# Performance work log

Measured on AMD Instinct MI355X. Metric: run time of the kernel, lower is better.

Reference implementation:

```python
import jax, jax.numpy as jnp
import numpy as np

B, S, IN, HID, HEADS, TRAITS = 128, 32, 32, 128, 8, 10


def setup_inputs() -> dict:
    key = jax.random.key(0)
    ks = jax.random.split(key, 40)
    f32 = jnp.float32
    def W(k, shape, s=0.02):
        return (jax.random.normal(k, shape, f32) * s)
    path = jax.random.normal(ks[0], (B, S, IN), f32)
    # monotonically increasing shared time grid (timestamps[0] is what cdeint uses)
    dt = jax.random.uniform(ks[1], (S,), f32, 0.05, 0.15)
    ts = jnp.broadcast_to(jnp.cumsum(dt), (B, S))
    inp = {
        "interaction_path": path,
        "timestamps": ts,
        # initial encoder: Linear(IN,HID) -> LN -> GELU -> Linear(HID,HID) -> LN
        "enc_W1": W(ks[2], (IN, HID)), "enc_b1": jnp.zeros((HID,), f32),
        "enc_g1": jnp.ones((HID,), f32), "enc_bt1": jnp.zeros((HID,), f32),
        "enc_W2": W(ks[3], (HID, HID)), "enc_b2": jnp.zeros((HID,), f32),
        "enc_g2": jnp.ones((HID,), f32), "enc_bt2": jnp.zeros((HID,), f32),
        # vector field: Linear(HID,2HID)->LN->GELU -> Linear(2HID,2HID)->LN->GELU -> Linear(2HID,HID*IN)
        "vf_W1": W(ks[4], (HID, 2 * HID)), "vf_b1": jnp.zeros((2 * HID,), f32),
        "vf_g1": jnp.ones((2 * HID,), f32), "vf_bt1": jnp.zeros((2 * HID,), f32),
        "vf_W2": W(ks[5], (2 * HID, 2 * HID)), "vf_b2": jnp.zeros((2 * HID,), f32),
        "vf_g2": jnp.ones((2 * HID,), f32), "vf_bt2": jnp.zeros((2 * HID,), f32),
        "vf_W3": W(ks[6], (2 * HID, HID * IN), 0.005), "vf_b3": jnp.zeros((HID * IN,), f32),
        # MultiheadAttention (q=k=v, single token)
        "Wq": W(ks[7], (HID, HID)), "bq": jnp.zeros((HID,), f32),
        "Wk": W(ks[8], (HID, HID)), "bk": jnp.zeros((HID,), f32),
        "Wv": W(ks[9], (HID, HID)), "bv": jnp.zeros((HID,), f32),
        "Wo": W(ks[10], (HID, HID)), "bo": jnp.zeros((HID,), f32),
        # trait decoder (2-layer MLP -> TRAITS)
        "dec_W1": W(ks[11], (HID, HID)), "dec_b1": jnp.zeros((HID,), f32),
        "dec_W2": W(ks[12], (HID, TRAITS)), "dec_b2": jnp.zeros((TRAITS,), f32),
    }
    return inp


def reference(interaction_path, timestamps,
              enc_W1, enc_b1, enc_g1, enc_bt1, enc_W2, enc_b2, enc_g2, enc_bt2,
              vf_W1, vf_b1, vf_g1, vf_bt1, vf_W2, vf_b2, vf_g2, vf_bt2, vf_W3, vf_b3,
              Wq, bq, Wk, bk, Wv, bv, Wo, bo,
              dec_W1, dec_b1, dec_W2, dec_b2):
    b, s, in_dim = interaction_path.shape
    hid = enc_W1.shape[1]
    nh = HEADS
    dh = hid // nh

    def ln(x, g, bb):
        mu = jnp.mean(x, -1, keepdims=True)
        v = jnp.mean((x - mu) ** 2, -1, keepdims=True)
        return (x - mu) / jnp.sqrt(v + 1e-5) * g + bb

    gelu = lambda x: jax.nn.gelu(x, approximate=False)

    # initial encoder on first time point (dropout = eval mode)
    x0 = interaction_path[:, 0]
    h0 = gelu(ln(x0 @ enc_W1 + enc_b1, enc_g1, enc_bt1))
    z0 = ln(h0 @ enc_W2 + enc_b2, enc_g2, enc_bt2)  # [B, HID]

    # linear-interpolation control path: piecewise-constant derivative per interval
    dts = timestamps[:, 1:] - timestamps[:, :-1]                       # [B, S-1]
    dX = (interaction_path[:, 1:] - interaction_path[:, :-1]) / dts[..., None]  # [B, S-1, IN]

    def vf(z):
        h = gelu(ln(z @ vf_W1 + vf_b1, vf_g1, vf_bt1))
        h = gelu(ln(h @ vf_W2 + vf_b2, vf_g2, vf_bt2))
        return (h @ vf_W3 + vf_b3).reshape(z.shape[0], hid, in_dim)    # [B, HID, IN]

    def drift(z, dxdt):
        return jnp.einsum('bhi,bi->bh', vf(z), dxdt)

    def rk4_step(z, inp):
        dxdt, hstep = inp               # [B, IN], [B]
        hb = hstep[:, None]
        k1 = drift(z, dxdt)
        k2 = drift(z + 0.5 * hb * k1, dxdt)
        k3 = drift(z + 0.5 * hb * k2, dxdt)
        k4 = drift(z + hb * k3, dxdt)
        z_next = z + (hb / 6.0) * (k1 + 2 * k2 + 2 * k3 + k4)
        return z_next, None

    zT, _ = jax.lax.scan(rk4_step, z0, (jnp.swapaxes(dX, 0, 1), dts.T))  # [B, HID]

    # single-token self-attention (softmax over one key -> weights = 1)
    q = (zT @ Wq + bq).reshape(b, nh, dh)
    k = (zT @ Wk + bk).reshape(b, nh, dh)
    v = (zT @ Wv + bv).reshape(b, nh, dh)
    scores = jnp.sum(q * k, -1, keepdims=True) / jnp.sqrt(jnp.float32(dh))  # [B, nh, 1]
    w = jax.nn.softmax(scores[..., None], axis=-1)                           # [B, nh, 1, 1] == 1
    attn = (w[..., 0] * v).reshape(b, hid)
    final = attn @ Wo + bo
    attention_weights = jnp.mean(w, axis=1)  # [B, 1, 1] averaged over heads (torch default)

    hD = gelu(final @ dec_W1 + dec_b1)
    traits = hD @ dec_W2 + dec_b2            # [B, TRAITS]
    return traits, attention_weights
```

## Files before the change

### kernel.cpp

```cpp
#include <hip/hip_runtime.h>
#include <hip/hip_bf16.h>

#define BB 128
#define SS 32
#define NSTEP 31
#define IND 32
#define HID 128
#define HID2 256

typedef unsigned short u16;
typedef unsigned int u32;
typedef _Float16 f16;
typedef f16 h2 __attribute__((ext_vector_type(2)));
typedef __fp16 fp16v2 __attribute__((ext_vector_type(2)));
typedef _Float16 f16x8 __attribute__((ext_vector_type(8)));
typedef float f32x4 __attribute__((ext_vector_type(4)));

__device__ __forceinline__ float dot2f(u32 a, u32 b, float c){
#if __has_builtin(__builtin_amdgcn_fdot2)
  h2 ha, hb; __builtin_memcpy(&ha, &a, 4); __builtin_memcpy(&hb, &b, 4);
  return __builtin_amdgcn_fdot2(ha, hb, c, false);
#else
  h2 ha, hb; __builtin_memcpy(&ha, &a, 4); __builtin_memcpy(&hb, &b, 4);
  return c + (float)ha[0]*(float)hb[0] + (float)ha[1]*(float)hb[1];
#endif
}
__device__ __forceinline__ u32 pkh2(float a, float b){
  fp16v2 r = __builtin_amdgcn_cvt_pkrtz(a, b);
  u32 u; __builtin_memcpy(&u, &r, 4); return u;
}
__device__ __forceinline__ u16 f2h(float f){ f16 h = (f16)f; u16 u; __builtin_memcpy(&u, &h, 2); return u; }
__device__ __forceinline__ float gelu_f(float x){ return 0.5f * x * (1.0f + erff(x * 0.70710678118654752440f)); }
__device__ __forceinline__ void setprio_hi(){
#if __has_builtin(__builtin_amdgcn_s_setprio)
  __builtin_amdgcn_s_setprio(3);
#endif
}
__device__ __forceinline__ void setprio_lo(){
#if __has_builtin(__builtin_amdgcn_s_setprio)
  __builtin_amdgcn_s_setprio(0);
#endif
}

__device__ __forceinline__ float wred(float v){
  int iv; float tf;
  #define DPPADD(CTRL, RMASK) \
    __builtin_memcpy(&iv, &v, 4); \
    iv = __builtin_amdgcn_update_dpp(0, iv, CTRL, RMASK, 0xf, true); \
    __builtin_memcpy(&tf, &iv, 4); \
    v += tf;
  DPPADD(0x111, 0xf)
  DPPADD(0x112, 0xf)
  DPPADD(0x114, 0xf)
  DPPADD(0x118, 0xf)
  DPPADD(0x142, 0xa)
  DPPADD(0x143, 0xc)
  #undef DPPADD
  return v;
}

__device__ __forceinline__ void bsum2(float x, float y, float* red, int tid, float& ox, float& oy){
  #pragma unroll
  for (int off = 32; off >= 1; off >>= 1){ x += __shfl_xor(x, off); y += __shfl_xor(y, off); }
  __syncthreads();
  if ((tid & 63) == 0){ red[(tid >> 6)*2] = x; red[(tid >> 6)*2 + 1] = y; }
  __syncthreads();
  ox = red[0] + red[2] + red[4] + red[6];
  oy = red[1] + red[3] + red[5] + red[7];
}

__global__ __launch_bounds__(256) void setup_kernel(const float* __restrict__ path,
                                                    const float* __restrict__ ts,
                                                    const float* __restrict__ b3,
                                                    const float* __restrict__ W3,
                                                    const float* __restrict__ W1,
                                                    const float* __restrict__ W2,
                                                    u32* __restrict__ dxh,
                                                    float* __restrict__ hb,
                                                    float* __restrict__ gb,
                                                    u32* __restrict__ w3h,
                                                    u32* __restrict__ w1f,
                                                    u32* __restrict__ w2f){
  const int blk = blockIdx.x, tid = threadIdx.x;
  if (blk < BB){
    const int b = blk;
    __shared__ float sdxp[NSTEP * IND];
    for (int t = tid; t < NSTEP * IND; t += 256){
      int s = t >> 5, i = t & 31;
      float dt = ts[b*SS + s + 1] - ts[b*SS + s];
      sdxp[t] = (path[(b*SS + s + 1)*IND + i] - path[(b*SS + s)*IND + i]) / dt;
    }
    if (tid < NSTEP) hb[b*NSTEP + tid] = ts[b*SS + tid + 1] - ts[b*SS + tid];
    __syncthreads();
    for (int t = tid; t < NSTEP * 16; t += 256){
      int s = t >> 4, i2 = t & 15;
      dxh[((size_t)b*NSTEP + s)*16 + i2] = pkh2(sdxp[s*IND + 2*i2], sdxp[s*IND + 2*i2 + 1]);
    }
    if (tid < HID){
      float w[IND];
      #pragma unroll
      for (int i = 0; i < IND; ++i) w[i] = b3[tid*IND + i];
      for (int s = 0; s < NSTEP; ++s){
        float a = 0.f;
        #pragma unroll
        for (int i = 0; i < IND; ++i) a = fmaf(w[i], sdxp[s*IND + i], a);
        gb[(b*NSTEP + s)*HID + tid] = a;
      }
    }
  } else if (blk < BB + 2048){
    int i = (blk - BB)*256 + tid;
    if (i < (HID2*HID*IND)/2) w3h[i] = pkh2(W3[2*i], W3[2*i + 1]);
  } else {
    int i = (blk - BB - 2048)*256 + tid;
    if (i < 16384){
      int lane_blk = i >> 6, rem = i & 63;
      int i16 = rem >> 2, q = rem & 3;
      int w = lane_blk >> 6, lane = lane_blk & 63;
      int kt = i16 >> 2, nt = i16 & 3;
      int k = kt*32 + (lane >> 4)*8 + 2*q;
      int col = w*64 + nt*16 + (lane & 15);
      w1f[i] = pkh2(W1[(size_t)k*HID2 + col], W1[(size_t)(k+1)*HID2 + col]);
    } else if (i < 16384 + 32768){
      int j = i - 16384;
      int lane_blk = j >> 7, rem = j & 127;
      int i32i = rem >> 2, q = rem & 3;
      int w = lane_blk >> 6, lane = lane_blk & 63;
      int kt = i32i >> 2, nt = i32i & 3;
      int k = kt*32 + (lane >> 4)*8 + 2*q;
      int col = w*64 + nt*16 + (lane & 15);
      w2f[j] = pkh2(W2[(size_t)k*HID2 + col], W2[(size_t)(k+1)*HID2 + col]);
    }
  }
}

struct FusedP {
  const float *path;
  const float *eW1,*eb1,*eg1,*ebt1,*eW2,*eb2,*eg2,*ebt2;
  const u32 *w1f, *w2f;
  const float *b1,*g1,*bt1,*b2,*g2,*bt2;
  const float *Wv,*bv,*Wo,*bo,*dW1,*db1,*dW2,*db2;
  const float *hb,*gb;
  const u32 *Gp;
  float *zstate, *out;
  int s0, s1, do_enc, do_epi, scan_on;
  const u32 *w3h, *dxh;
  u32 *Gpw;
  int ps0, pcs;
};

__global__ __launch_bounds__(256, 1) void fused_kernel(FusedP p){
  const int tid = threadIdx.x;
  __shared__ __align__(16) u16 zst_h[HID];
  __shared__ __align__(16) u16 a1p_h[HID2];
  __shared__ __align__(16) u16 a2p_h[HID2];
  __shared__ __align__(16) float red[8];
  __shared__ __align__(16) float zf[HID];
  __shared__ __align__(16) float sc1[HID2];
  __shared__ u32 sdx[BB * 16];

  if (p.scan_on && blockIdx.x < BB){
    setprio_hi();
    const int b = blockIdx.x;
    const int lane = tid & 63, w = tid >> 6;
    const int quad = lane >> 4, n16 = lane & 15;
    const bool owner = (quad == 0);

    uint4 w1r[16], w2r[32];
    {
      const uint4* s1p = (const uint4*)p.w1f + ((size_t)(w*64 + lane))*16;
      #pragma unroll
      for (int i = 0; i < 16; ++i) w1r[i] = s1p[i];
      const uint4* s2p = (const uint4*)p.w2f + ((size_t)(w*64 + lane))*32;
      #pragma unroll
      for (int i = 0; i < 32; ++i) w2r[i] = s2p[i];
    }
    float rb1[4], rg1[4], rbt1[4], rb2[4], rg2[4], rbt2[4];
    #pragma unroll
    for (int nt = 0; nt < 4; ++nt){
      int col = w*64 + nt*16 + n16;
      rb1[nt] = p.b1[col]; rg1[nt] = p.g1[col]; rbt1[nt] = p.bt1[col];
      rb2[nt] = p.b2[col]; rg2[nt] = p.g2[col]; rbt2[nt] = p.bt2[col];
    }
    const int h0 = w*32 + n16, h1 = h0 + 16;

    float mu, sq;
    if (p.do_enc){
      if (tid < IND) sc1[tid] = p.path[(b*SS + 0)*IND + tid];
      __syncthreads();
      float acc = 0.f;
      if (tid < HID){
        acc = p.eb1[tid];
        #pragma unroll 8
        for (int i = 0; i < IND; ++i) acc = fmaf(sc1[i], p.eW1[i*HID + tid], acc);
      }
      float cx = (tid < HID) ? acc : 0.f;
      bsum2(cx, cx*cx, red, tid, mu, sq);
      mu *= (1.f/HID); float var = sq*(1.f/HID) - mu*mu; float rstd = rsqrtf(var + 1e-5f);
      if (tid < HID) zf[tid] = gelu_f((acc - mu)*rstd*p.eg1[tid] + p.ebt1[tid]);
      __syncthreads();
      float acc2 = 0.f;
      if (tid < HID){
        acc2 = p.eb2[tid];
        #pragma unroll 8
        for (int h = 0; h < HID; ++h) acc2 = fmaf(zf[h], p.eW2[h*HID + tid], acc2);
      }
      cx = (tid < HID) ? acc2 : 0.f;
      bsum2(cx, cx*cx, red, tid, mu, sq);
      mu *= (1.f/HID); float var2 = sq*(1.f/HID) - mu*mu; float rstd2 = rsqrtf(var2 + 1e-5f);
      __syncthreads();
      if (tid < HID) zf[tid] = (acc2 - mu)*rstd2*p.eg2[tid] + p.ebt2[tid];
      __syncthreads();
    }
    float zc0 = 0.f, zc1 = 0.f;
    if (owner){
      if (p.do_enc){ zc0 = zf[h0]; zc1 = zf[h1]; }
      else { zc0 = p.zstate[b*HID + h0]; zc1 = p.zstate[b*HID + h1]; }
    }

    for (int s = p.s0; s < p.s1; ++s){
      const float hbv = p.hb[b*NSTEP + s];
      uint4 gr[16];
      {
        const uint4* g4 = (const uint4*)(p.Gp + ((size_t)(s - p.s0)*BB + b)*16384 + (size_t)w*4096);
        #pragma unroll
        for (int m = 0; m < 16; ++m) gr[m] = g4[m*64 + lane];
      }
      float gb0 = 0.f, gb1 = 0.f;
      if (owner){
        gb0 = p.gb[(b*NSTEP + s)*HID + h0];
        gb1 = p.gb[(b*NSTEP + s)*HID + h1];
        zst_h[h0] = f2h(zc0); zst_h[h1] = f2h(zc1);
      }
      float ks0 = 0.f, ks1 = 0.f;
      __syncthreads();

      #pragma unroll 1
      for (int st = 0; st < 4; ++st){
        f32x4 D0a={0,0,0,0}, D1a={0,0,0,0}, D2a={0,0,0,0}, D3a={0,0,0,0};
        f32x4 D0b={0,0,0,0}, D1b={0,0,0,0}, D2b={0,0,0,0}, D3b={0,0,0,0};
        {
          const uint4* za = (const uint4*)zst_h;
          #pragma unroll
          for (int kt = 0; kt < 2; ++kt){
            f16x8 a; uint4 av = za[kt*4 + quad]; __builtin_memcpy(&a, &av, 16);
            f16x8 bf;
            __builtin_memcpy(&bf, &w1r[kt*4+0], 16); D0a = __builtin_amdgcn_mfma_f32_16x16x32_f16(a, bf, D0a, 0, 0, 0);
            __builtin_memcpy(&bf, &w1r[kt*4+1], 16); D1a = __builtin_amdgcn_mfma_f32_16x16x32_f16(a, bf, D1a, 0, 0, 0);
            __builtin_memcpy(&bf, &w1r[kt*4+2], 16); D2a = __builtin_amdgcn_mfma_f32_16x16x32_f16(a, bf, D2a, 0, 0, 0);
            __builtin_memcpy(&bf, &w1r[kt*4+3], 16); D3a = __builtin_amdgcn_mfma_f32_16x16x32_f16(a, bf, D3a, 0, 0, 0);
          }
          #pragma unroll
          for (int kt = 2; kt < 4; ++kt){
            f16x8 a; uint4 av = za[kt*4 + quad]; __builtin_memcpy(&a, &av, 16);
            f16x8 bf;
            __builtin_memcpy(&bf, &w1r[kt*4+0], 16); D0b = __builtin_amdgcn_mfma_f32_16x16x32_f16(a, bf, D0b, 0, 0, 0);
            __builtin_memcpy(&bf, &w1r[kt*4+1], 16); D1b = __builtin_amdgcn_mfma_f32_16x16x32_f16(a, bf, D1b, 0, 0, 0);
            __builtin_memcpy(&bf, &w1r[kt*4+2], 16); D2b = __builtin_amdgcn_mfma_f32_16x16x32_f16(a, bf, D2b, 0, 0, 0);
            __builtin_memcpy(&bf, &w1r[kt*4+3], 16); D3b = __builtin_amdgcn_mfma_f32_16x16x32_f16(a, bf, D3b, 0, 0, 0);
          }
        }
        float v0 = (D0a[0]+D0b[0]) + rb1[0], v1 = (D1a[0]+D1b[0]) + rb1[1];
        float v2 = (D2a[0]+D2b[0]) + rb1[2], v3 = (D3a[0]+D3b[0]) + rb1[3];
        float ssum = wred((v0 + v1) + (v2 + v3));
        float ssq  = wred((v0*v0 + v1*v1) + (v2*v2 + v3*v3));
        if (lane == 63){ red[w*2] = ssum; red[w*2+1] = ssq; }
        __syncthreads();
        {
          const float4* r4 = (const float4*)red;
          float4 ra = r4[0], rb = r4[1];
          float m1 = (ra.x + ra.z + rb.x + rb.z)*(1.f/1024.f);
          float q1 = (ra.y + ra.w + rb.y + rb.w)*(1.f/1024.f);
          float rs1 = rsqrtf(q1 - m1*m1 + 1e-5f);
          if (owner){
            a1p_h[w*64 +  0 + n16] = f2h(gelu_f((v0 - m1)*rs1*rg1[0] + rbt1[0]));
            a1p_h[w*64 + 16 + n16] = f2h(gelu_f((v1 - m1)*rs1*rg1[1] + rbt1[1]));
            a1p_h[w*64 + 32 + n16] = f2h(gelu_f((v2 - m1)*rs1*rg1[2] + rbt1[2]));
            a1p_h[w*64 + 48 + n16] = f2h(gelu_f((v3 - m1)*rs1*rg1[3] + rbt1[3]));
          }
        }
        __syncthreads();
        D0a={0,0,0,0}; D1a={0,0,0,0}; D2a={0,0,0,0}; D3a={0,0,0,0};
        D0b={0,0,0,0}; D1b={0,0,0,0}; D2b={0,0,0,0}; D3b={0,0,0,0};
        {
          const uint4* aa = (const uint4*)a1p_h;
          #pragma unroll
          for (int kt = 0; kt < 4; ++kt){
            f16x8 a; uint4 av = aa[kt*4 + quad]; __builtin_memcpy(&a, &av, 16);
            f16x8 bf;
            __builtin_memcpy(&bf, &w2r[kt*4+0], 16); D0a = __builtin_amdgcn_mfma_f32_16x16x32_f16(a, bf, D0a, 0, 0, 0);
            __builtin_memcpy(&bf, &w2r[kt*4+1], 16); D1a = __builtin_amdgcn_mfma_f32_16x16x32_f16(a, bf, D1a, 0, 0, 0);
            __builtin_memcpy(&bf, &w2r[kt*4+2], 16); D2a = __builtin_amdgcn_mfma_f32_16x16x32_f16(a, bf, D2a, 0, 0, 0);
            __builtin_memcpy(&bf, &w2r[kt*4+3], 16); D3a = __builtin_amdgcn_mfma_f32_16x16x32_f16(a, bf, D3a, 0, 0, 0);
          }
          #pragma unroll
          for (int kt = 4; kt < 8; ++kt){
            f16x8 a; uint4 av = aa[kt*4 + quad]; __builtin_memcpy(&a, &av, 16);
            f16x8 bf;
            __builtin_memcpy(&bf, &w2r[kt*4+0], 16); D0b = __builtin_amdgcn_mfma_f32_16x16x32_f16(a, bf, D0b, 0, 0, 0);
            __builtin_memcpy(&bf, &w2r[kt*4+1], 16); D1b = __builtin_amdgcn_mfma_f32_16x16x32_f16(a, bf, D1b, 0, 0, 0);
            __builtin_memcpy(&bf, &w2r[kt*4+2], 16); D2b = __builtin_amdgcn_mfma_f32_16x16x32_f16(a, bf, D2b, 0, 0, 0);
            __builtin_memcpy(&bf, &w2r[kt*4+3], 16); D3b = __builtin_amdgcn_mfma_f32_16x16x32_f16(a, bf, D3b, 0, 0, 0);
          }
        }
        v0 = (D0a[0]+D0b[0]) + rb2[0]; v1 = (D1a[0]+D1b[0]) + rb2[1];
        v2 = (D2a[0]+D2b[0]) + rb2[2]; v3 = (D3a[0]+D3b[0]) + rb2[3];
        ssum = wred((v0 + v1) + (v2 + v3));
        ssq  = wred((v0*v0 + v1*v1) + (v2*v2 + v3*v3));
        if (lane == 63){ red[w*2] = ssum; red[w*2+1] = ssq; }
        __syncthreads();
        {
          const float4* r4 = (const float4*)red;
          float4 ra = r4[0], rb = r4[1];
          float m2 = (ra.x + ra.z + rb.x + rb.z)*(1.f/1024.f);
          float q2 = (ra.y + ra.w + rb.y + rb.w)*(1.f/1024.f);
          float rs2 = rsqrtf(q2 - m2*m2 + 1e-5f);
          if (owner){
            a2p_h[w*64 +  0 + n16] = f2h(gelu_f((v0 - m2)*rs2*rg2[0] + rbt2[0]));
            a2p_h[w*64 + 16 + n16] = f2h(gelu_f((v1 - m2)*rs2*rg2[1] + rbt2[1]));
            a2p_h[w*64 + 32 + n16] = f2h(gelu_f((v2 - m2)*rs2*rg2[2] + rbt2[2]));
            a2p_h[w*64 + 48 + n16] = f2h(gelu_f((v3 - m2)*rs2*rg2[3] + rbt2[3]));
          }
        }
        __syncthreads();
        f32x4 E0={0,0,0,0}, E1={0,0,0,0}, E2={0,0,0,0}, E3={0,0,0,0};
        {
          const uint4* aa = (const uint4*)a2p_h;
          #pragma unroll
          for (int kt = 0; kt < 4; ++kt){
            f16x8 a; uint4 av = aa[kt*4 + quad]; __builtin_memcpy(&a, &av, 16);
            f16x8 g0f, g1f;
            __builtin_memcpy(&g0f, &gr[kt*2+0], 16);
            __builtin_memcpy(&g1f, &gr[kt*2+1], 16);
            E0 = __builtin_amdgcn_mfma_f32_16x16x32_f16(a, g0f, E0, 0, 0, 0);
            E1 = __builtin_amdgcn_mfma_f32_16x16x32_f16(a, g1f, E1, 0, 0, 0);
          }
          #pragma unroll
          for (int kt = 4; kt < 8; ++kt){
            f16x8 a; uint4 av = aa[kt*4 + quad]; __builtin_memcpy(&a, &av, 16);
            f16x8 g0f, g1f;
            __builtin_memcpy(&g0f, &gr[kt*2+0], 16);
            __builtin_memcpy(&g1f, &gr[kt*2+1], 16);
            E2 = __builtin_amdgcn_mfma_f32_16x16x32_f16(a, g0f, E2, 0, 0, 0);
            E3 = __builtin_amdgcn_mfma_f32_16x16x32_f16(a, g1f, E3, 0, 0, 0);
          }
        }
        if (owner){
          float kv0 = (E0[0] + E2[0]) + gb0, kv1 = (E1[0] + E3[0]) + gb1;
          float cst = (st == 0 || st == 3) ? 1.f : 2.f;
          ks0 += cst*kv0; ks1 += cst*kv1;
          if (st < 3){
            float c = (st == 2) ? hbv : 0.5f*hbv;
            zst_h[h0] = f2h(zc0 + c*kv0);
            zst_h[h1] = f2h(zc1 + c*kv1);
          }
        }
        __syncthreads();
      }
      if (owner){ zc0 += hbv*(1.f/6.f)*ks0; zc1 += hbv*(1.f/6.f)*ks1; }
    }

    if (p.do_epi){
      if (owner){ zf[h0] = zc0; zf[h1] = zc1; }
      __syncthreads();
      if (tid < HID){
        float v = p.bv[tid];
        #pragma unroll 8
        for (int h = 0; h < HID; ++h) v = fmaf(zf[h], p.Wv[h*HID + tid], v);
        sc1[tid] = v;
      }
      __syncthreads();
      if (tid < HID){
        float f = p.bo[tid];
        #pragma unroll 8
        for (int h = 0; h < HID; ++h) f = fmaf(sc1[h], p.Wo[h*HID + tid], f);
        sc1[HID + tid] = f;
      }
      __syncthreads();
      if (tid < HID){
        float hd = p.db1[tid];
        #pragma unroll 8
        for (int h = 0; h < HID; ++h) hd = fmaf(sc1[HID + h], p.dW1[h*HID + tid], hd);
        zf[tid] = gelu_f(hd);
      }
      __syncthreads();
      if (tid < 10){
        float t = p.db2[tid];
        #pragma unroll 8
        for (int h = 0; h < HID; ++h) t = fmaf(zf[h], p.dW2[h*10 + tid], t);
        p.out[b*10 + tid] = t;
      }
      if (tid == 0) p.out[BB*10 + b] = 1.0f;
    } else {
      if (owner){ p.zstate[b*HID + h0] = zc0; p.zstate[b*HID + h1] = zc1; }
    }
    return;
  }

  {
    setprio_lo();
    const int pb = blockIdx.x - (p.scan_on ? BB : 0);
    const int sl = pb >> 6, xblk = pb & 63;
    if (sl >= p.pcs) return;
    const int s = p.ps0 + sl;
    const int lin = xblk*256 + tid;
    const int kp = lin >> 7, h = lin & 127;
    const uint4* wa = (const uint4*)(p.w3h + ((size_t)(2*kp)*HID + h)*16);
    const uint4* wb = (const uint4*)(p.w3h + ((size_t)(2*kp+1)*HID + h)*16);
    uint4 A0 = wa[0], A1 = wa[1], A2 = wa[2], A3 = wa[3];
    uint4 B0 = wb[0], B1 = wb[1], B2 = wb[2], B3 = wb[3];
    for (int t = tid; t < BB * 16; t += 256){
      int bb = t >> 4, i2 = t & 15;
      sdx[t] = p.dxh[((size_t)bb*NSTEP + s)*16 + i2];
    }
    __syncthreads();
    const int kt = kp >> 4, q = kp & 3, quad2 = (kp >> 2) & 3;
    const int wq = h >> 5, tq = (h >> 4) & 1, nn = h & 15;
    const size_t off = (size_t)wq*4096 + (size_t)(kt*2 + tq)*256 + (size_t)(quad2*16 + nn)*4 + q;
    const size_t base_sl = (size_t)sl * BB * 16384;
    u32* __restrict__ Gout = p.Gpw;
    for (int bb = 0; bb < BB; ++bb){
      const uint4* dp = (const uint4*)&sdx[bb*16];
      uint4 D0 = dp[0], D1 = dp[1], D2 = dp[2], D3 = dp[3];
      float g0 = 0.f, g1 = 0.f, g2 = 0.f, g3 = 0.f;
      g0 = dot2f(D0.x, A0.x, g0); g0 = dot2f(D0.y, A0.y, g0);
      g0 = dot2f(D0.z, A0.z, g0); g0 = dot2f(D0.w, A0.w, g0);
      g2 = dot2f(D1.x, A1.x, g2); g2 = dot2f(D1.y, A1.y, g2);
      g2 = dot2f(D1.z, A1.z, g2); g2 = dot2f(D1.w, A1.w, g2);
      g0 = dot2f(D2.x, A2.x, g0); g0 = dot2f(D2.y, A2.y, g0);
      g0 = dot2f(D2.z, A2.z, g0); g0 = dot2f(D2.w, A2.w, g0);
      g2 = dot2f(D3.x, A3.x, g2); g2 = dot2f(D3.y, A3.y, g2);
      g2 = dot2f(D3.z, A3.z, g2); g2 = dot2f(D3.w, A3.w, g2);
      g1 = dot2f(D0.x, B0.x, g1); g1 = dot2f(D0.y, B0.y, g1);
      g1 = dot2f(D0.z, B0.z, g1); g1 = dot2f(D0.w, B0.w, g1);
      g3 = dot2f(D1.x, B1.x, g3); g3 = dot2f(D1.y, B1.y, g3);
      g3 = dot2f(D1.z, B1.z, g3); g3 = dot2f(D1.w, B1.w, g3);
      g1 = dot2f(D2.x, B2.x, g1); g1 = dot2f(D2.y, B2.y, g1);
      g1 = dot2f(D2.z, B2.z, g1); g1 = dot2f(D2.w, B2.w, g1);
      g3 = dot2f(D3.x, B3.x, g3); g3 = dot2f(D3.y, B3.y, g3);
      g3 = dot2f(D3.z, B3.z, g3); g3 = dot2f(D3.w, B3.w, g3);
      Gout[base_sl + (size_t)bb*16384 + off] = pkh2(g0 + g2, g1 + g3);
    }
  }
}

extern "C" void kernel_launch(void* const* d_in, const int* in_sizes, int n_in,
                              void* d_out, int out_size, void* d_ws, size_t ws_size,
                              hipStream_t stream){
  const float* path  = (const float*)d_in[0];
  const float* ts    = (const float*)d_in[1];
  const float* eW1   = (const float*)d_in[2];
  const float* eb1   = (const float*)d_in[3];
  const float* eg1   = (const float*)d_in[4];
  const float* ebt1  = (const float*)d_in[5];
  const float* eW2   = (const float*)d_in[6];
  const float* eb2   = (const float*)d_in[7];
  const float* eg2   = (const float*)d_in[8];
  const float* ebt2  = (const float*)d_in[9];
  const float* vW1   = (const float*)d_in[10];
  const float* vb1   = (const float*)d_in[11];
  const float* vg1   = (const float*)d_in[12];
  const float* vbt1  = (const float*)d_in[13];
  const float* vW2   = (const float*)d_in[14];
  const float* vb2   = (const float*)d_in[15];
  const float* vg2   = (const float*)d_in[16];
  const float* vbt2  = (const float*)d_in[17];
  const float* vW3   = (const float*)d_in[18];
  const float* vb3   = (const float*)d_in[19];
  const float* Wv    = (const float*)d_in[24];
  const float* bv    = (const float*)d_in[25];
  const float* Wo    = (const float*)d_in[26];
  const float* bo    = (const float*)d_in[27];
  const float* dW1   = (const float*)d_in[28];
  const float* db1   = (const float*)d_in[29];
  const float* dW2   = (const float*)d_in[30];
  const float* db2   = (const float*)d_in[31];

  char* wsb = (char*)d_ws;
  float* z_state = (float*)(wsb + 0);
  u32*   dxh = (u32*)(wsb + 65536);
  float* hb  = (float*)(wsb + 319488);
  float* gb  = (float*)(wsb + 335872);
  u32*   w3h = (u32*)(wsb + 2367488);
  u32*   w1f = (u32*)(wsb + 4464640);
  u32*   w2f = (u32*)(wsb + 4530176);
  const size_t gbase = 4661248;

  hipLaunchKernelGGL(setup_kernel, dim3(BB + 2048 + 192), dim3(256), 0, stream,
                     path, ts, vb3, vW3, vW1, vW2, dxh, hb, gb, w3h, w1f, w2f);

  const size_t per_step = (size_t)BB * 16384 * 4;
  size_t avail = (ws_size > gbase) ? (ws_size - gbase) : 0;
  int cap = (int)((avail/2) / per_step);

  FusedP base;
  base.path = path;
  base.eW1 = eW1; base.eb1 = eb1; base.eg1 = eg1; base.ebt1 = ebt1;
  base.eW2 = eW2; base.eb2 = eb2; base.eg2 = eg2; base.ebt2 = ebt2;
  base.w1f = w1f; base.w2f = w2f;
  base.b1 = vb1; base.g1 = vg1; base.bt1 = vbt1;
  base.b2 = vb2; base.g2 = vg2; base.bt2 = vbt2;
  base.Wv = Wv; base.bv = bv; base.Wo = Wo; base.bo = bo;
  base.dW1 = dW1; base.db1 = db1; base.dW2 = dW2; base.db2 = db2;
  base.hb = hb; base.gb = gb;
  base.zstate = z_state; base.out = (float*)d_out;
  base.w3h = w3h; base.dxh = dxh;
  base.s0 = 0; base.s1 = 0; base.do_enc = 0; base.do_epi = 0; base.scan_on = 0;
  base.ps0 = 0; base.pcs = 0;

  if (cap >= 2){
    int c = cap < 8 ? cap : 8;
    if (c > NSTEP) c = NSTEP;
    const int nch = (NSTEP + c - 1) / c;
    u32* GpA = (u32*)(wsb + gbase);
    u32* GpB = (u32*)(wsb + gbase + (size_t)c*per_step);
    for (int i = 0; i <= nch; ++i){
      FusedP P = base;
      int scan_i = i - 1, prep_i = i;
      P.scan_on = (scan_i >= 0) ? 1 : 0;
      if (P.scan_on){
        P.s0 = scan_i*c;
        P.s1 = (P.s0 + c < NSTEP) ? (P.s0 + c) : NSTEP;
        P.Gp = (scan_i & 1) ? GpB : GpA;
        P.do_enc = (scan_i == 0) ? 1 : 0;
        P.do_epi = (P.s1 == NSTEP) ? 1 : 0;
      } else {
        P.Gp = GpA;
      }
      if (prep_i < nch){
        P.ps0 = prep_i*c;
        P.pcs = (NSTEP - P.ps0 < c) ? (NSTEP - P.ps0) : c;
        P.Gpw = (prep_i & 1) ? GpB : GpA;
      } else {
        P.pcs = 0; P.Gpw = GpA;
      }
      int grid = (P.scan_on ? BB : 0) + 64*P.pcs;
      if (grid == 0) continue;
      hipLaunchKernelGGL(fused_kernel, dim3(grid), dim3(256), 0, stream, P);
    }
  } else {
    int c = (int)(avail / per_step);
    if (c < 1) c = 1;
    if (c > NSTEP) c = NSTEP;
    u32* GpA = (u32*)(wsb + gbase);
    const int nch = (NSTEP + c - 1) / c;
    for (int i = 0; i < nch; ++i){
      int s0 = i*c;
      int cs = (NSTEP - s0 < c) ? (NSTEP - s0) : c;
      FusedP P1 = base;
      P1.scan_on = 0; P1.ps0 = s0; P1.pcs = cs; P1.Gpw = GpA; P1.Gp = GpA;
      hipLaunchKernelGGL(fused_kernel, dim3(64*cs), dim3(256), 0, stream, P1);
      FusedP P2 = base;
      P2.scan_on = 1; P2.pcs = 0; P2.Gpw = GpA;
      P2.s0 = s0; P2.s1 = s0 + cs; P2.Gp = GpA;
      P2.do_enc = (s0 == 0) ? 1 : 0;
      P2.do_epi = (s0 + cs == NSTEP) ? 1 : 0;
      hipLaunchKernelGGL(fused_kernel, dim3(BB), dim3(256), 0, stream, P2);
    }
  }
}
```

Measured before the change: 525.0 us.

## Fold first-chunk G precompute into setup kernel to drop a launch

The setup kernel gains extra blocks that compute the first chunk's projected vector-field table directly from fp32 W3 and the path differences, writing into buffer A. The pipeline loop then starts at the first scan chunk, so the prep-only launch is gone and its work overlaps with the weight-conversion blocks. The cost is a larger static shared-memory allocation for every setup block, which may lower occupancy, plus duplicate fp32 math on W3. Numerics can differ slightly from the fp16 path.

```diff
diff --git a/kernel.cpp b/kernel.cpp
--- a/kernel.cpp
+++ b/kernel.cpp
@@ -80,11 +80,14 @@
                                                     float* __restrict__ gb,
                                                     u32* __restrict__ w3h,
                                                     u32* __restrict__ w1f,
-                                                    u32* __restrict__ w2f){
+                                                    u32* __restrict__ w2f,
+                                                    u32* __restrict__ Gp0,
+                                                    int pcs0){
   const int blk = blockIdx.x, tid = threadIdx.x;
+  __shared__ float sdxp[NSTEP * IND];
+  __shared__ __align__(16) float sdxf[BB * IND];
   if (blk < BB){
     const int b = blk;
-    __shared__ float sdxp[NSTEP * IND];
     for (int t = tid; t < NSTEP * IND; t += 256){
       int s = t >> 5, i = t & 31;
       float dt = ts[b*SS + s + 1] - ts[b*SS + s];
@@ -110,7 +113,7 @@
   } else if (blk < BB + 2048){
     int i = (blk - BB)*256 + tid;
     if (i < (HID2*HID*IND)/2) w3h[i] = pkh2(W3[2*i], W3[2*i + 1]);
-  } else {
+  } else if (blk < BB + 2048 + 192){
     int i = (blk - BB - 2048)*256 + tid;
     if (i < 16384){
       int lane_blk = i >> 6, rem = i & 63;
@@ -129,6 +132,49 @@
       int k = kt*32 + (lane >> 4)*8 + 2*q;
       int col = w*64 + nt*16 + (lane & 15);
       w2f[j] = pkh2(W2[(size_t)k*HID2 + col], W2[(size_t)(k+1)*HID2 + col]);
+    }
+  } else {
+    const int pb = blk - (BB + 2048 + 192);
+    const int sl = pb >> 6, xblk = pb & 63;
+    if (sl >= pcs0) return;
+    const int s = sl;
+    const int lin = xblk*256 + tid;
+    const int kp = lin >> 7, h = lin & 127;
+    const float* wra = W3 + (size_t)(2*kp)*4096 + h*IND;
+    const float* wrb = wra + 4096;
+    float4 A[8], Bv[8];
+    #pragma unroll
+    for (int i = 0; i < 8; ++i){ A[i] = ((const float4*)wra)[i]; Bv[i] = ((const float4*)wrb)[i]; }
+    for (int t = tid; t < BB * IND; t += 256){
+      int bb = t >> 5, i = t & 31;
+      float dt = ts[bb*SS + s + 1] - ts[bb*SS + s];
+      sdxf[t] = (path[((size_t)bb*SS + s + 1)*IND + i] - path[((size_t)bb*SS + s)*IND + i]) / dt;
+    }
+    __syncthreads();
+    const int kt = kp >> 4, q = kp & 3, quad2 = (kp >> 2) & 3;
+    const int wq = h >> 5, tq = (h >> 4) & 1, nn = h & 15;
+    const size_t off = (size_t)wq*4096 + (size_t)(kt*2 + tq)*256 + (size_t)(quad2*16 + nn)*4 + q;
+    u32* __restrict__ Gout = Gp0 + (size_t)sl * BB * 16384;
+    for (int bb = 0; bb < BB; ++bb){
+      const float4* dp = (const float4*)&sdxf[bb*IND];
+      float e0 = 0.f, e1 = 0.f, o0 = 0.f, o1 = 0.f;
+      #pragma unroll
+      for (int i = 0; i < 4; ++i){
+        float4 d = dp[i];
+        e0 = fmaf(d.x, A[i].x, e0);  e0 = fmaf(d.y, A[i].y, e0);
+        e0 = fmaf(d.z, A[i].z, e0);  e0 = fmaf(d.w, A[i].w, e0);
+        o0 = fmaf(d.x, Bv[i].x, o0); o0 = fmaf(d.y, Bv[i].y, o0);
+        o0 = fmaf(d.z, Bv[i].z, o0); o0 = fmaf(d.w, Bv[i].w, o0);
+      }
+      #pragma unroll
+      for (int i = 4; i < 8; ++i){
+        float4 d = dp[i];
+        e1 = fmaf(d.x, A[i].x, e1);  e1 = fmaf(d.y, A[i].y, e1);
+        e1 = fmaf(d.z, A[i].z, e1);  e1 = fmaf(d.w, A[i].w, e1);
+        o1 = fmaf(d.x, Bv[i].x, o1); o1 = fmaf(d.y, Bv[i].y, o1);
+        o1 = fmaf(d.z, Bv[i].z, o1); o1 = fmaf(d.w, Bv[i].w, o1);
+      }
+      Gout[(size_t)bb*16384 + off] = pkh2(e0 + e1, o0 + o1);
     }
   }
 }
@@ -485,9 +531,6 @@
   u32*   w2f = (u32*)(wsb + 4530176);
   const size_t gbase = 4661248;
 
-  hipLaunchKernelGGL(setup_kernel, dim3(BB + 2048 + 192), dim3(256), 0, stream,
-                     path, ts, vb3, vW3, vW1, vW2, dxh, hb, gb, w3h, w1f, w2f);
-
   const size_t per_step = (size_t)BB * 16384 * 4;
   size_t avail = (ws_size > gbase) ? (ws_size - gbase) : 0;
   int cap = (int)((avail/2) / per_step);
@@ -513,19 +556,19 @@
     const int nch = (NSTEP + c - 1) / c;
     u32* GpA = (u32*)(wsb + gbase);
     u32* GpB = (u32*)(wsb + gbase + (size_t)c*per_step);
-    for (int i = 0; i <= nch; ++i){
+
+    hipLaunchKernelGGL(setup_kernel, dim3(BB + 2048 + 192 + 64*c), dim3(256), 0, stream,
+                       path, ts, vb3, vW3, vW1, vW2, dxh, hb, gb, w3h, w1f, w2f, GpA, c);
+
+    for (int i = 1; i <= nch; ++i){
       FusedP P = base;
       int scan_i = i - 1, prep_i = i;
-      P.scan_on = (scan_i >= 0) ? 1 : 0;
-      if (P.scan_on){
-        P.s0 = scan_i*c;
-        P.s1 = (P.s0 + c < NSTEP) ? (P.s0 + c) : NSTEP;
-        P.Gp = (scan_i & 1) ? GpB : GpA;
-        P.do_enc = (scan_i == 0) ? 1 : 0;
-        P.do_epi = (P.s1 == NSTEP) ? 1 : 0;
-      } else {
-        P.Gp = GpA;
-      }
+      P.scan_on = 1;
+      P.s0 = scan_i*c;
+      P.s1 = (P.s0 + c < NSTEP) ? (P.s0 + c) : NSTEP;
+      P.Gp = (scan_i & 1) ? GpB : GpA;
+      P.do_enc = (scan_i == 0) ? 1 : 0;
+      P.do_epi = (P.s1 == NSTEP) ? 1 : 0;
       if (prep_i < nch){
         P.ps0 = prep_i*c;
         P.pcs = (NSTEP - P.ps0 < c) ? (NSTEP - P.ps0) : c;
@@ -533,11 +576,12 @@
       } else {
         P.pcs = 0; P.Gpw = GpA;
       }
-      int grid = (P.scan_on ? BB : 0) + 64*P.pcs;
-      if (grid == 0) continue;
+      int grid = BB + 64*P.pcs;
       hipLaunchKernelGGL(fused_kernel, dim3(grid), dim3(256), 0, stream, P);
     }
   } else {
+    hipLaunchKernelGGL(setup_kernel, dim3(BB + 2048 + 192), dim3(256), 0, stream,
+                       path, ts, vb3, vW3, vW1, vW2, dxh, hb, gb, w3h, w1f, w2f, (u32*)(wsb + gbase), 0);
     int c = (int)(avail / per_step);
     if (c < 1) c = 1;
     if (c > NSTEP) c = NSTEP;
```

After: 537.4 us. 1.02x slower.
